# Kernel tuning notes

Hardware: AMD Instinct MI355X
Metric: run time of the kernel (lower is better)

## Reference

```python
import jax, jax.numpy as jnp
import numpy as np

B, D, rL, rD, d = 512, 960, 16, 32, 512
LP, LH = 16, 384
R_PH = 0.7
dP = int(round(R_PH * d))  # 358
dH = d - dP                # 154
BN_EPS = 1e-5


def _xavier(key, shape):
    limit = float(np.sqrt(6.0 / (shape[0] + shape[1])))
    return jax.random.uniform(key, shape, jnp.float32, -limit, limit)


def _prefix_mask(key, batch, L_pad):
    # contiguous prefix masks: Lb uniform in [1, L_pad]
    lens = jax.random.randint(key, (batch,), 1, L_pad + 1)
    return (jnp.arange(L_pad)[None, :] < lens[:, None]).astype(jnp.int32)


def setup_inputs() -> dict:
    key = jax.random.key(0)
    ks = jax.random.split(key, 24)
    inp = {
        "emb_P": jax.random.normal(ks[0], (B, LP, D), jnp.float32),
        "emb_H": jax.random.normal(ks[1], (B, LH, D), jnp.float32),
        "mask_P": _prefix_mask(ks[2], B, LP),
        "mask_H": _prefix_mask(ks[3], B, LH),
        # peptide encoder params
        "B_cP": _xavier(ks[4], (D, rD)),
        "A_cP": _xavier(ks[5], (LP, rL)),
        "H_cP": _xavier(ks[6], (rL * rD, dP)),
        "W1P": _xavier(ks[7], (dP, dP)), "b1P": jnp.zeros((dP,), jnp.float32),
        "gP": jnp.ones((dP,), jnp.float32), "betaP": jnp.zeros((dP,), jnp.float32),
        "W2P": _xavier(ks[8], (dP, dP)), "b2P": jnp.zeros((dP,), jnp.float32),
        # HLA encoder params
        "B_cH": _xavier(ks[9], (D, rD)),
        "A_cH": _xavier(ks[10], (LH, rL)),
        "H_cH": _xavier(ks[11], (rL * rD, dH)),
        "W1H": _xavier(ks[12], (dH, dH)), "b1H": jnp.zeros((dH,), jnp.float32),
        "gH": jnp.ones((dH,), jnp.float32), "betaH": jnp.zeros((dH,), jnp.float32),
        "W2H": _xavier(ks[13], (dH, dH)), "b2H": jnp.zeros((dH,), jnp.float32),
    }
    return inp


def _encode(emb, mask, B_c, A_c, H_c, W1, b1, g, beta, W2, b2):
    # masked low-rank projection; equivalent to the per-sample ragged loop
    # for contiguous prefix masks (A_c rows align with padded positions).
    Xm = emb * mask[..., None].astype(emb.dtype)            # (B, L, D)
    Y = jnp.einsum("bld,dr->blr", Xm, B_c)                  # (B, L, rD)
    U = jnp.einsum("lp,blr->bpr", A_c, Y)                   # (B, rL, rD)
    z = U.reshape(U.shape[0], -1) @ H_c                     # (B, d_mod)
    # expander (eval mode: BN uses running stats mean=0/var=1; dropout off)
    h = z @ W1 + b1
    h = h * (g / jnp.sqrt(1.0 + BN_EPS)) + beta
    h = jax.nn.relu(h)
    return h @ W2 + b2


def reference(emb_P, emb_H, B_cP, A_cP, H_cP, W1P, b1P, gP, betaP, W2P, b2P,
              B_cH, A_cH, H_cH, W1H, b1H, gH, betaH, W2H, b2H,
              mask_P, mask_H):
    zP = _encode(emb_P, mask_P, B_cP, A_cP, H_cP, W1P, b1P, gP, betaP, W2P, b2P)
    zH = _encode(emb_H, mask_H, B_cH, A_cH, H_cH, W1H, b1H, gH, betaH, W2H, b2H)
    return jnp.concatenate([zP, zH], axis=-1)  # (B, d)
```

## Files before the change

kernel.cpp:

```cpp
#include <hip/hip_runtime.h>
#include <cstddef>

constexpr int Bn  = 512;
constexpr int Dd  = 960;
constexpr int RL  = 16;
constexpr int RD  = 32;
constexpr int LPp = 16;
constexpr int LHh = 384;
constexpr int DP  = 358;
constexpr int DH  = 154;

typedef float f32x4 __attribute__((ext_vector_type(4)));

struct EncParams {
    const float* X;
    const int*   mask;
    const float* A;
    const float* Bc;
    const float* Hc;
    const float* W1; const float* b1; const float* g; const float* beta;
    const float* W2; const float* b2;
    int L, dmod, ooff;
};

__global__ void zero_kernel(int* __restrict__ q)
{
    if (threadIdx.x == 0) *q = 0;
}

__global__ __launch_bounds__(256)
void persist_kernel(EncParams H, EncParams P, int* __restrict__ qcnt,
                    float* __restrict__ out)
{
    const int t = threadIdx.x;
    __shared__ float Vs[RL][Dd];
    __shared__ float Ush[RL * RD];
    __shared__ int   s_item, s_len;

    for (;;) {
        __syncthreads();
        if (t == 0) { s_item = atomicAdd(qcnt, 1); s_len = 0; }
        __syncthreads();
        const int item = s_item;
        if (item >= 2 * Bn) return;
        const bool isH = (item < Bn);
        const EncParams E = isH ? H : P;
        const int b = isH ? item : item - Bn;

        int loc = 0;
        for (int i = t; i < E.L; i += 256) loc += E.mask[(size_t)b * E.L + i];
        if (loc) atomicAdd(&s_len, loc);
        __syncthreads();
        const int len = s_len;

        if (t < 240) {
            float v[RL][4];
            #pragma unroll
            for (int p = 0; p < RL; ++p)
                #pragma unroll
                for (int q = 0; q < 4; ++q) v[p][q] = 0.f;

            const float* xrow = E.X + (size_t)b * E.L * Dd + 4 * t;
            int l = 0;
            for (; l + 1 < len; l += 2) {
                f32x4 xv0 = __builtin_nontemporal_load((const f32x4*)xrow);
                f32x4 xv1 = __builtin_nontemporal_load((const f32x4*)(xrow + Dd));
                xrow += 2 * Dd;
                float a0[RL], a1[RL];
                *(f32x4*)&a0[0]  = *(const f32x4*)(E.A + (size_t)l * RL + 0);
                *(f32x4*)&a0[4]  = *(const f32x4*)(E.A + (size_t)l * RL + 4);
                *(f32x4*)&a0[8]  = *(const f32x4*)(E.A + (size_t)l * RL + 8);
                *(f32x4*)&a0[12] = *(const f32x4*)(E.A + (size_t)l * RL + 12);
                *(f32x4*)&a1[0]  = *(const f32x4*)(E.A + (size_t)(l + 1) * RL + 0);
                *(f32x4*)&a1[4]  = *(const f32x4*)(E.A + (size_t)(l + 1) * RL + 4);
                *(f32x4*)&a1[8]  = *(const f32x4*)(E.A + (size_t)(l + 1) * RL + 8);
                *(f32x4*)&a1[12] = *(const f32x4*)(E.A + (size_t)(l + 1) * RL + 12);
                #pragma unroll
                for (int p = 0; p < RL; ++p) {
                    #pragma unroll
                    for (int q = 0; q < 4; ++q)
                        v[p][q] = fmaf(a0[p], xv0[q], v[p][q]);
                }
                #pragma unroll
                for (int p = 0; p < RL; ++p) {
                    #pragma unroll
                    for (int q = 0; q < 4; ++q)
                        v[p][q] = fmaf(a1[p], xv1[q], v[p][q]);
                }
            }
            if (l < len) {
                f32x4 xv = __builtin_nontemporal_load((const f32x4*)xrow);
                float a[RL];
                *(f32x4*)&a[0]  = *(const f32x4*)(E.A + (size_t)l * RL + 0);
                *(f32x4*)&a[4]  = *(const f32x4*)(E.A + (size_t)l * RL + 4);
                *(f32x4*)&a[8]  = *(const f32x4*)(E.A + (size_t)l * RL + 8);
                *(f32x4*)&a[12] = *(const f32x4*)(E.A + (size_t)l * RL + 12);
                #pragma unroll
                for (int p = 0; p < RL; ++p)
                    #pragma unroll
                    for (int q = 0; q < 4; ++q)
                        v[p][q] = fmaf(a[p], xv[q], v[p][q]);
            }
            #pragma unroll
            for (int p = 0; p < RL; ++p)
                *(f32x4*)&Vs[p][4 * t] = *(f32x4*)&v[p][0];
        }
        __syncthreads();

        {
            const int p = t >> 5, r = t & 31;
            float u0 = 0.f, u1 = 0.f;
            for (int dd = 0; dd < Dd; dd += 4) {
                f32x4 v0 = *(const f32x4*)&Vs[p][dd];
                f32x4 v1 = *(const f32x4*)&Vs[p + 8][dd];
                #pragma unroll
                for (int q = 0; q < 4; ++q) {
                    float bc = E.Bc[(size_t)(dd + q) * RD + r];
                    u0 = fmaf(v0[q], bc, u0);
                    u1 = fmaf(v1[q], bc, u1);
                }
            }
            Ush[p * RD + r]       = u0;
            Ush[(p + 8) * RD + r] = u1;
        }
        __syncthreads();

        float* zs = &Vs[0][0];
        float* hs = &Vs[0][0] + 512;
        for (int j = t; j < E.dmod; j += 256) {
            float acc0 = 0.f, acc1 = 0.f;
            #pragma unroll 8
            for (int i = 0; i < RL * RD; i += 2) {
                acc0 = fmaf(Ush[i],     E.Hc[(size_t)i * E.dmod + j],       acc0);
                acc1 = fmaf(Ush[i + 1], E.Hc[(size_t)(i + 1) * E.dmod + j], acc1);
            }
            zs[j] = acc0 + acc1;
        }
        __syncthreads();

        const float bscale = rsqrtf(1.f + 1e-5f);
        for (int c = t; c < E.dmod; c += 256) {
            float acc = E.b1[c];
            #pragma unroll 4
            for (int k = 0; k < E.dmod; ++k)
                acc = fmaf(zs[k], E.W1[(size_t)k * E.dmod + c], acc);
            acc = fmaf(acc, E.g[c] * bscale, E.beta[c]);
            hs[c] = fmaxf(acc, 0.f);
        }
        __syncthreads();

        for (int c = t; c < E.dmod; c += 256) {
            float acc = E.b2[c];
            #pragma unroll 4
            for (int k = 0; k < E.dmod; ++k)
                acc = fmaf(hs[k], E.W2[(size_t)k * E.dmod + c], acc);
            out[(size_t)b * (DP + DH) + E.ooff + c] = acc;
        }
    }
}

extern "C" void kernel_launch(void* const* d_in, const int* in_sizes, int n_in,
                              void* d_out, int out_size, void* d_ws, size_t ws_size,
                              hipStream_t stream)
{
    EncParams P, H;
    P.X    = (const float*)d_in[0];
    H.X    = (const float*)d_in[1];
    P.mask = (const int*)  d_in[2];
    H.mask = (const int*)  d_in[3];
    P.Bc   = (const float*)d_in[4];
    P.A    = (const float*)d_in[5];
    P.Hc   = (const float*)d_in[6];
    P.W1   = (const float*)d_in[7];
    P.b1   = (const float*)d_in[8];
    P.g    = (const float*)d_in[9];
    P.beta = (const float*)d_in[10];
    P.W2   = (const float*)d_in[11];
    P.b2   = (const float*)d_in[12];
    H.Bc   = (const float*)d_in[13];
    H.A    = (const float*)d_in[14];
    H.Hc   = (const float*)d_in[15];
    H.W1   = (const float*)d_in[16];
    H.b1   = (const float*)d_in[17];
    H.g    = (const float*)d_in[18];
    H.beta = (const float*)d_in[19];
    H.W2   = (const float*)d_in[20];
    H.b2   = (const float*)d_in[21];
    P.L = LPp;  P.dmod = DP;  P.ooff = 0;
    H.L = LHh;  H.dmod = DH;  H.ooff = DP;

    float* outp = (float*)d_out;
    int*   qcnt = (int*)d_ws;

    zero_kernel<<<dim3(1), dim3(64), 0, stream>>>(qcnt);
    persist_kernel<<<dim3(512), dim3(256), 0, stream>>>(H, P, qcnt, outp);
}
```

Baseline: 256.2 us.

## Chunk sequence loop with LDS-staged A and double-buffered 8-row X prefetch

The per-row loop over valid positions becomes a chunked loop (64 rows for H, 16 for P). Each chunk stages its A_c rows in shared memory, zero-padded past the valid length, and the thread keeps two banks of 8 X-row vector loads in flight while computing on the other bank. The aim is more memory-level parallelism on the dominant X stream. The cost is reading padded X rows up to the chunk boundary and holding more registers. The later Bc, Hc, W1 and W2 reductions also split into multiple independent accumulators to shorten FMA dependency chains.

```diff
diff --git a/kernel.cpp b/kernel.cpp
--- a/kernel.cpp
+++ b/kernel.cpp
@@ -34,6 +34,7 @@
 {
     const int t = threadIdx.x;
     __shared__ float Vs[RL][Dd];
+    __shared__ float As[64 * RL];
     __shared__ float Ush[RL * RD];
     __shared__ int   s_item, s_len;
 
@@ -46,6 +47,7 @@
         const bool isH = (item < Bn);
         const EncParams E = isH ? H : P;
         const int b = isH ? item : item - Bn;
+        const int CH = isH ? 64 : 16;
 
         int loc = 0;
         for (int i = t; i < E.L; i += 256) loc += E.mask[(size_t)b * E.L + i];
@@ -53,54 +55,70 @@
         __syncthreads();
         const int len = s_len;
 
+        float v[RL][4];
+        #pragma unroll
+        for (int p = 0; p < RL; ++p)
+            #pragma unroll
+            for (int q = 0; q < 4; ++q) v[p][q] = 0.f;
+
+        const float* Xb = E.X + (size_t)b * E.L * Dd + 4 * t;
+
+        for (int c0 = 0; c0 < len; c0 += CH) {
+            __syncthreads();
+            if (4 * t < CH * RL) {
+                const int row = c0 + (t >> 2);
+                f32x4 av = {0.f, 0.f, 0.f, 0.f};
+                if (row < len)
+                    av = *(const f32x4*)(E.A + (size_t)row * RL + (t & 3) * 4);
+                *(f32x4*)&As[4 * t] = av;
+            }
+            __syncthreads();
+
+            if (t < 240) {
+                auto computeOct = [&](int r0, f32x4* x) {
+                    #pragma unroll
+                    for (int rr = 0; rr < 8; ++rr) {
+                        float a[RL];
+                        *(f32x4*)&a[0]  = *(const f32x4*)&As[(r0 + rr) * RL + 0];
+                        *(f32x4*)&a[4]  = *(const f32x4*)&As[(r0 + rr) * RL + 4];
+                        *(f32x4*)&a[8]  = *(const f32x4*)&As[(r0 + rr) * RL + 8];
+                        *(f32x4*)&a[12] = *(const f32x4*)&As[(r0 + rr) * RL + 12];
+                        #pragma unroll
+                        for (int p = 0; p < RL; ++p) {
+                            v[p][0] = fmaf(a[p], x[rr][0], v[p][0]);
+                            v[p][1] = fmaf(a[p], x[rr][1], v[p][1]);
+                            v[p][2] = fmaf(a[p], x[rr][2], v[p][2]);
+                            v[p][3] = fmaf(a[p], x[rr][3], v[p][3]);
+                        }
+                    }
+                };
+                const int nocts = CH >> 3;
+                const float* base = Xb + (size_t)c0 * Dd;
+                f32x4 xa[8], xb[8];
+                #pragma unroll
+                for (int rr = 0; rr < 8; ++rr)
+                    xa[rr] = __builtin_nontemporal_load(
+                        (const f32x4*)(base + (size_t)rr * Dd));
+                for (int oc = 0; oc < nocts; oc += 2) {
+                    const float* pb = base + (size_t)(oc + 1) * 8 * Dd;
+                    #pragma unroll
+                    for (int rr = 0; rr < 8; ++rr)
+                        xb[rr] = __builtin_nontemporal_load(
+                            (const f32x4*)(pb + (size_t)rr * Dd));
+                    computeOct(oc * 8, xa);
+                    if (oc + 2 < nocts) {
+                        const float* pa = base + (size_t)(oc + 2) * 8 * Dd;
+                        #pragma unroll
+                        for (int rr = 0; rr < 8; ++rr)
+                            xa[rr] = __builtin_nontemporal_load(
+                                (const f32x4*)(pa + (size_t)rr * Dd));
+                    }
+                    computeOct((oc + 1) * 8, xb);
+                }
+            }
+        }
+        __syncthreads();
         if (t < 240) {
-            float v[RL][4];
-            #pragma unroll
-            for (int p = 0; p < RL; ++p)
-                #pragma unroll
-                for (int q = 0; q < 4; ++q) v[p][q] = 0.f;
-
-            const float* xrow = E.X + (size_t)b * E.L * Dd + 4 * t;
-            int l = 0;
-            for (; l + 1 < len; l += 2) {
-                f32x4 xv0 = __builtin_nontemporal_load((const f32x4*)xrow);
-                f32x4 xv1 = __builtin_nontemporal_load((const f32x4*)(xrow + Dd));
-                xrow += 2 * Dd;
-                float a0[RL], a1[RL];
-                *(f32x4*)&a0[0]  = *(const f32x4*)(E.A + (size_t)l * RL + 0);
-                *(f32x4*)&a0[4]  = *(const f32x4*)(E.A + (size_t)l * RL + 4);
-                *(f32x4*)&a0[8]  = *(const f32x4*)(E.A + (size_t)l * RL + 8);
-                *(f32x4*)&a0[12] = *(const f32x4*)(E.A + (size_t)l * RL + 12);
-                *(f32x4*)&a1[0]  = *(const f32x4*)(E.A + (size_t)(l + 1) * RL + 0);
-                *(f32x4*)&a1[4]  = *(const f32x4*)(E.A + (size_t)(l + 1) * RL + 4);
-                *(f32x4*)&a1[8]  = *(const f32x4*)(E.A + (size_t)(l + 1) * RL + 8);
-                *(f32x4*)&a1[12] = *(const f32x4*)(E.A + (size_t)(l + 1) * RL + 12);
-                #pragma unroll
-                for (int p = 0; p < RL; ++p) {
-                    #pragma unroll
-                    for (int q = 0; q < 4; ++q)
-                        v[p][q] = fmaf(a0[p], xv0[q], v[p][q]);
-                }
-                #pragma unroll
-                for (int p = 0; p < RL; ++p) {
-                    #pragma unroll
-                    for (int q = 0; q < 4; ++q)
-                        v[p][q] = fmaf(a1[p], xv1[q], v[p][q]);
-                }
-            }
-            if (l < len) {
-                f32x4 xv = __builtin_nontemporal_load((const f32x4*)xrow);
-                float a[RL];
-                *(f32x4*)&a[0]  = *(const f32x4*)(E.A + (size_t)l * RL + 0);
-                *(f32x4*)&a[4]  = *(const f32x4*)(E.A + (size_t)l * RL + 4);
-                *(f32x4*)&a[8]  = *(const f32x4*)(E.A + (size_t)l * RL + 8);
-                *(f32x4*)&a[12] = *(const f32x4*)(E.A + (size_t)l * RL + 12);
-                #pragma unroll
-                for (int p = 0; p < RL; ++p)
-                    #pragma unroll
-                    for (int q = 0; q < 4; ++q)
-                        v[p][q] = fmaf(a[p], xv[q], v[p][q]);
-            }
             #pragma unroll
             for (int p = 0; p < RL; ++p)
                 *(f32x4*)&Vs[p][4 * t] = *(f32x4*)&v[p][0];
@@ -109,52 +127,65 @@
 
         {
             const int p = t >> 5, r = t & 31;
-            float u0 = 0.f, u1 = 0.f;
-            for (int dd = 0; dd < Dd; dd += 4) {
-                f32x4 v0 = *(const f32x4*)&Vs[p][dd];
-                f32x4 v1 = *(const f32x4*)&Vs[p + 8][dd];
+            float u00 = 0.f, u01 = 0.f, u10 = 0.f, u11 = 0.f;
+            for (int dd = 0; dd < Dd; dd += 8) {
+                f32x4 v0a = *(const f32x4*)&Vs[p][dd];
+                f32x4 v0b = *(const f32x4*)&Vs[p][dd + 4];
+                f32x4 v1a = *(const f32x4*)&Vs[p + 8][dd];
+                f32x4 v1b = *(const f32x4*)&Vs[p + 8][dd + 4];
                 #pragma unroll
                 for (int q = 0; q < 4; ++q) {
-                    float bc = E.Bc[(size_t)(dd + q) * RD + r];
-                    u0 = fmaf(v0[q], bc, u0);
-                    u1 = fmaf(v1[q], bc, u1);
+                    float bca = E.Bc[(size_t)(dd + q) * RD + r];
+                    float bcb = E.Bc[(size_t)(dd + 4 + q) * RD + r];
+                    u00 = fmaf(v0a[q], bca, u00);
+                    u01 = fmaf(v0b[q], bcb, u01);
+                    u10 = fmaf(v1a[q], bca, u10);
+                    u11 = fmaf(v1b[q], bcb, u11);
                 }
             }
-            Ush[p * RD + r]       = u0;
-            Ush[(p + 8) * RD + r] = u1;
+            Ush[p * RD + r]       = u00 + u01;
+            Ush[(p + 8) * RD + r] = u10 + u11;
         }
         __syncthreads();
 
         float* zs = &Vs[0][0];
         float* hs = &Vs[0][0] + 512;
         for (int j = t; j < E.dmod; j += 256) {
-            float acc0 = 0.f, acc1 = 0.f;
-            #pragma unroll 8
-            for (int i = 0; i < RL * RD; i += 2) {
-                acc0 = fmaf(Ush[i],     E.Hc[(size_t)i * E.dmod + j],       acc0);
-                acc1 = fmaf(Ush[i + 1], E.Hc[(size_t)(i + 1) * E.dmod + j], acc1);
-            }
-            zs[j] = acc0 + acc1;
+            float a0 = 0.f, a1 = 0.f, a2 = 0.f, a3 = 0.f;
+            #pragma unroll 4
+            for (int i = 0; i < RL * RD; i += 4) {
+                a0 = fmaf(Ush[i],     E.Hc[(size_t)i * E.dmod + j],       a0);
+                a1 = fmaf(Ush[i + 1], E.Hc[(size_t)(i + 1) * E.dmod + j], a1);
+                a2 = fmaf(Ush[i + 2], E.Hc[(size_t)(i + 2) * E.dmod + j], a2);
+                a3 = fmaf(Ush[i + 3], E.Hc[(size_t)(i + 3) * E.dmod + j], a3);
+            }
+            zs[j] = (a0 + a1) + (a2 + a3);
         }
         __syncthreads();
 
         const float bscale = rsqrtf(1.f + 1e-5f);
-        for (int c = t; c < E.dmod; c += 256) {
-            float acc = E.b1[c];
+        const int K = E.dmod;
+        for (int c = t; c < K; c += 256) {
+            float a0 = E.b1[c], a1 = 0.f;
             #pragma unroll 4
-            for (int k = 0; k < E.dmod; ++k)
-                acc = fmaf(zs[k], E.W1[(size_t)k * E.dmod + c], acc);
+            for (int k = 0; k < K; k += 2) {
+                a0 = fmaf(zs[k],     E.W1[(size_t)k * K + c],       a0);
+                a1 = fmaf(zs[k + 1], E.W1[(size_t)(k + 1) * K + c], a1);
+            }
+            float acc = a0 + a1;
             acc = fmaf(acc, E.g[c] * bscale, E.beta[c]);
             hs[c] = fmaxf(acc, 0.f);
         }
         __syncthreads();
 
-        for (int c = t; c < E.dmod; c += 256) {
-            float acc = E.b2[c];
+        for (int c = t; c < K; c += 256) {
+            float a0 = E.b2[c], a1 = 0.f;
             #pragma unroll 4
-            for (int k = 0; k < E.dmod; ++k)
-                acc = fmaf(hs[k], E.W2[(size_t)k * E.dmod + c], acc);
-            out[(size_t)b * (DP + DH) + E.ooff + c] = acc;
+            for (int k = 0; k < K; k += 2) {
+                a0 = fmaf(hs[k],     E.W2[(size_t)k * K + c],       a0);
+                a1 = fmaf(hs[k + 1], E.W2[(size_t)(k + 1) * K + c], a1);
+            }
+            out[(size_t)b * (DP + DH) + E.ooff + c] = a0 + a1;
         }
     }
 }
```

After: 342.8 us. +33.8%, slower.
